# Kernel tuning notes

Measured on AMD Instinct MI355X. Metric: run time of the kernel, lower is better.

The kernel has to match this reference:

```python
import jax, jax.numpy as jnp
import numpy as np

D_MODEL = 1024
NUM_HEADS = 16
D_K = D_MODEL // NUM_HEADS
D_FF = 4096
THETA = 10000.0
EPS = 1e-5
B, S = 4, 2048


def _trunc_normal(key, shape, fan_in, fan_out):
    std = (2.0 / (fan_in + fan_out)) ** 0.5
    return jax.random.truncated_normal(key, -3.0, 3.0, shape, jnp.float32) * std


def setup_inputs() -> dict:
    key = jax.random.key(0)
    ks = jax.random.split(key, 8)
    return {
        "x": jax.random.normal(ks[0], (B, S, D_MODEL), jnp.float32),
        "wq": _trunc_normal(ks[1], (D_MODEL, D_MODEL), D_MODEL, D_MODEL),
        "wk": _trunc_normal(ks[2], (D_MODEL, D_MODEL), D_MODEL, D_MODEL),
        "wv": _trunc_normal(ks[3], (D_MODEL, D_MODEL), D_MODEL, D_MODEL),
        "wo": _trunc_normal(ks[4], (D_MODEL, D_MODEL), D_MODEL, D_MODEL),
        "g1": jnp.ones((D_MODEL,), jnp.float32),
        "g2": jnp.ones((D_MODEL,), jnp.float32),
        "w1": _trunc_normal(ks[5], (D_FF, D_MODEL), D_MODEL, D_FF),
        "w2": _trunc_normal(ks[6], (D_MODEL, D_FF), D_FF, D_MODEL),
        "w3": _trunc_normal(ks[7], (D_FF, D_MODEL), D_MODEL, D_FF),
    }


def _rmsnorm(x, g):
    rms = jnp.sqrt(jnp.mean(x * x, axis=-1, keepdims=True) + EPS)
    return x / rms * g


def _rope(x):
    # x: [b, h, s, d_k], interleaved rotary embedding
    s = x.shape[-2]
    inv_freq = 1.0 / (THETA ** (jnp.arange(0, D_K, 2, dtype=jnp.float32) / D_K))
    angles = jnp.arange(s, dtype=jnp.float32)[:, None] * inv_freq  # [s, d_k/2]
    cos, sin = jnp.cos(angles), jnp.sin(angles)
    x1, x2 = x[..., ::2], x[..., 1::2]
    rot = jnp.stack([x1 * cos - x2 * sin, x1 * sin + x2 * cos], axis=-1)
    return rot.reshape(x.shape)


def reference(x, wq, wk, wv, wo, g1, g2, w1, w2, w3):
    b, s, _ = x.shape
    h, dk = NUM_HEADS, D_K

    # --- attention sublayer ---
    xn = _rmsnorm(x, g1)
    q = (xn @ wq.T).reshape(b, s, h, dk).transpose(0, 2, 1, 3)
    k = (xn @ wk.T).reshape(b, s, h, dk).transpose(0, 2, 1, 3)
    v = (xn @ wv.T).reshape(b, s, h, dk).transpose(0, 2, 1, 3)
    q, k = _rope(q), _rope(k)

    scores = jnp.einsum("bhqd,bhkd->bhqk", q, k) / (dk ** 0.5)
    causal = jnp.tril(jnp.ones((s, s), dtype=bool))
    scores = jnp.where(causal, scores, -1e9)
    attn = jax.nn.softmax(scores, axis=-1)
    ctx = jnp.einsum("bhqk,bhkd->bhqd", attn, v)
    ctx = ctx.transpose(0, 2, 1, 3).reshape(b, s, h * dk)
    y = x + ctx @ wo.T

    # --- SwiGLU FFN sublayer ---
    yn = _rmsnorm(y, g2)
    a = yn @ w1.T
    ff = (a * jax.nn.sigmoid(a)) * (yn @ w3.T)
    return y + ff @ w2.T
```

## Files before the change

### kernel.cpp

```cpp
#include <hip/hip_runtime.h>
#include <hip/hip_bf16.h>

typedef unsigned short u16;
typedef unsigned int u32;
typedef __bf16 bf16_8 __attribute__((ext_vector_type(8)));
typedef float f32x4 __attribute__((ext_vector_type(4)));

#define DEV __device__ __forceinline__

static const int T_TOK = 8192;
static const int DM    = 1024;
static const int SEQ   = 2048;

DEV u16 f2b(float f) {
  union { float f; u32 u; } v; v.f = f;
  u32 r = v.u + 0x7fffu + ((v.u >> 16) & 1u);
  return (u16)(r >> 16);
}
DEV float b2f(u16 b) {
  union { u32 u; float f; } v; v.u = ((u32)b) << 16;
  return v.f;
}
DEV void gload16(void* lds, const void* g) {
  __builtin_amdgcn_global_load_lds((const __attribute__((address_space(1))) u32*)g,
                                   (__attribute__((address_space(3))) u32*)lds, 16, 0, 0);
}
DEV void vmdrain() { asm volatile("s_waitcnt vmcnt(0)" ::: "memory"); }
DEV uint2 tr_read(u32 addr) {
  uint2 r;
  asm volatile("ds_read_b64_tr_b16 %0, %1" : "=v"(r) : "v"(addr));
  return r;
}

__global__ void cvt_bf16(const float* __restrict__ in, u16* __restrict__ out, int n) {
  int i = (blockIdx.x * blockDim.x + threadIdx.x) * 4;
  if (i >= n) return;
  float4 v = *(const float4*)(in + i);
  union { u16 h[4]; uint2 u; } pk;
  pk.h[0] = f2b(v.x); pk.h[1] = f2b(v.y); pk.h[2] = f2b(v.z); pk.h[3] = f2b(v.w);
  *(uint2*)(out + i) = pk.u;
}

__launch_bounds__(256)
__global__ void rmsnorm_k(const float* __restrict__ x, const float* __restrict__ g,
                          u16* __restrict__ out) {
  const int row = blockIdx.x;
  const float4 v = ((const float4*)(x + (size_t)row * DM))[threadIdx.x];
  float ss = v.x*v.x + v.y*v.y + v.z*v.z + v.w*v.w;
  #pragma unroll
  for (int off = 1; off < 64; off <<= 1) ss += __shfl_xor(ss, off, 64);
  __shared__ float ws[4];
  if ((threadIdx.x & 63) == 0) ws[threadIdx.x >> 6] = ss;
  __syncthreads();
  float tot = ws[0] + ws[1] + ws[2] + ws[3];
  float inv = rsqrtf(tot * (1.0f / DM) + 1e-5f);
  const float4 gv = ((const float4*)g)[threadIdx.x];
  union { u16 h[4]; uint2 u; } pk;
  pk.h[0] = f2b(v.x * inv * gv.x);
  pk.h[1] = f2b(v.y * inv * gv.y);
  pk.h[2] = f2b(v.z * inv * gv.z);
  pk.h[3] = f2b(v.w * inv * gv.w);
  *(uint2*)(out + (size_t)row * DM + threadIdx.x * 4) = pk.u;
}

__global__ void rope_k(u16* __restrict__ buf, float scale) {
  int idx = blockIdx.x * blockDim.x + threadIdx.x;
  if (idx >= T_TOK * 512) return;
  int t = idx >> 9;
  int p = idx & 511;
  int d = p & 31;
  int s = t & (SEQ - 1);
  float inv = __expf(-(float)d * (logf(10000.0f) / 32.0f));
  float ang = (float)s * inv;
  float sn = sinf(ang), cs = cosf(ang);
  size_t off = (size_t)t * DM + (size_t)(p >> 5) * 64 + 2 * d;
  float x1 = b2f(buf[off]), x2 = b2f(buf[off + 1]);
  buf[off]     = f2b((x1 * cs - x2 * sn) * scale);
  buf[off + 1] = f2b((x1 * sn + x2 * cs) * scale);
}

template<int MODE>
__launch_bounds__(256)
__global__ void gemm_nt(const u16* __restrict__ A, const u16* __restrict__ B,
                        u16* Cb, float* __restrict__ Cf,
                        const float* __restrict__ resid, const u16* aux,
                        int N, int K) {
  __shared__ __attribute__((aligned(16))) u16 As[128 * 32];
  __shared__ __attribute__((aligned(16))) u16 Bs[128 * 32];
  const int tid = threadIdx.x;
  const int w = tid >> 6, l = tid & 63;
  const int wr = w >> 1, wc = w & 1;
  const int nwg = gridDim.x * gridDim.y;
  const int id  = blockIdx.y * gridDim.x + blockIdx.x;
  const int nid = (id & 7) * (nwg >> 3) + (id >> 3);
  const int bx = nid % gridDim.x, by = nid / gridDim.x;
  const int brow = by * 128;
  const int bcol = bx * 128;
  const int lr = l & 15, lg = l >> 4, lk = lg * 8;
  f32x4 acc[4][4] = {};

  for (int kk = 0; kk < K; kk += 32) {
    {
      int c = tid;
      gload16((char*)As + (size_t)w * 1024,
              A + (size_t)(brow + (c >> 2)) * K + kk + (c & 3) * 8);
      gload16((char*)Bs + (size_t)w * 1024,
              B + (size_t)(bcol + (c >> 2)) * K + kk + (c & 3) * 8);
      c = tid + 256;
      gload16((char*)As + 4096 + (size_t)w * 1024,
              A + (size_t)(brow + (c >> 2)) * K + kk + (c & 3) * 8);
      gload16((char*)Bs + 4096 + (size_t)w * 1024,
              B + (size_t)(bcol + (c >> 2)) * K + kk + (c & 3) * 8);
    }
    vmdrain();
    __syncthreads();
    bf16_8 af[4], bf[4];
    #pragma unroll
    for (int m = 0; m < 4; ++m)
      af[m] = *(const bf16_8*)&As[(wr * 64 + m * 16 + lr) * 32 + lk];
    #pragma unroll
    for (int n = 0; n < 4; ++n)
      bf[n] = *(const bf16_8*)&Bs[(wc * 64 + n * 16 + lr) * 32 + lk];
    #pragma unroll
    for (int m = 0; m < 4; ++m)
      #pragma unroll
      for (int n = 0; n < 4; ++n)
        acc[m][n] = __builtin_amdgcn_mfma_f32_16x16x32_bf16(af[m], bf[n], acc[m][n], 0, 0, 0);
    __syncthreads();
  }

  #pragma unroll
  for (int m = 0; m < 4; ++m) {
    #pragma unroll
    for (int n = 0; n < 4; ++n) {
      #pragma unroll
      for (int r = 0; r < 4; ++r) {
        int row = brow + wr * 64 + m * 16 + lg * 4 + r;
        int col = bcol + wc * 64 + n * 16 + lr;
        size_t idx = (size_t)row * N + col;
        float v = acc[m][n][r];
        if (MODE == 0) {
          Cb[idx] = f2b(v);
        } else if (MODE == 1 || MODE == 3) {
          Cf[idx] = resid[idx] + v;
        } else if (MODE == 2) {
          float av = b2f(aux[idx]);
          float sig = 1.0f / (1.0f + __expf(-av));
          Cb[idx] = f2b(av * sig * v);
        }
      }
    }
  }
}

__launch_bounds__(256)
__global__ void attn_k(const u16* __restrict__ Q, const u16* __restrict__ Kb,
                       const u16* __restrict__ V, u16* __restrict__ CTX) {
  __shared__ __attribute__((aligned(16))) u16 Ks[64 * 64];
  __shared__ __attribute__((aligned(16))) u16 Vs[64 * 64];
  __shared__ __attribute__((aligned(16))) u16 Ps[4][16 * 64];
  const int tid = threadIdx.x, w = tid >> 6, l = tid & 63;
  const int bh = blockIdx.y;
  const int b = bh >> 4, h = bh & 15;
  const int lr = l & 15, lg = l >> 4;
  const size_t base = (size_t)b * SEQ * DM + (size_t)h * 64;
  const u32 vs_base = (u32)(size_t)&Vs[0];

  #pragma unroll 1
  for (int pass = 0; pass < 2; ++pass) {
    const int qt = pass ? (31 - blockIdx.x) : blockIdx.x;
    const int q0 = qt * 64;

    const size_t qrow = base + (size_t)(q0 + w * 16 + lr) * DM;
    bf16_8 qf0 = *(const bf16_8*)&Q[qrow + lg * 8];
    bf16_8 qf1 = *(const bf16_8*)&Q[qrow + 32 + lg * 8];

    f32x4 o[4] = {};
    float mrow[4], lsum[4];
    #pragma unroll
    for (int r = 0; r < 4; ++r) { mrow[r] = -3.0e38f; lsum[r] = 0.0f; }

    for (int kv0 = 0; kv0 < q0 + 64; kv0 += 64) {
      __syncthreads();
      {
        int u = tid, row = u >> 3, slot = u & 7;
        gload16((char*)Ks + (size_t)w * 1024,
                Kb + base + (size_t)(kv0 + row) * DM + ((slot * 8) ^ ((row & 7) << 3)));
        u = tid + 256; row = u >> 3; slot = u & 7;
        gload16((char*)Ks + 4096 + (size_t)w * 1024,
                Kb + base + (size_t)(kv0 + row) * DM + ((slot * 8) ^ ((row & 7) << 3)));
        u = tid;
        int kv = ((u >> 5) << 2) + ((u >> 1) & 3);
        int d  = (((u >> 3) & 3) << 4) + ((u & 1) << 3);
        gload16((char*)Vs + (size_t)w * 1024,
                V + base + (size_t)(kv0 + kv) * DM + d);
        u = tid + 256;
        kv = ((u >> 5) << 2) + ((u >> 1) & 3);
        d  = (((u >> 3) & 3) << 4) + ((u & 1) << 3);
        gload16((char*)Vs + 4096 + (size_t)w * 1024,
                V + base + (size_t)(kv0 + kv) * DM + d);
      }
      vmdrain();
      __syncthreads();

      f32x4 s[4];
      #pragma unroll
      for (int h0 = 0; h0 < 4; ++h0) {
        const int row = h0 * 16 + lr;
        bf16_8 k0 = *(const bf16_8*)&Ks[row * 64 + ((lg * 8) ^ ((lr & 7) << 3))];
        bf16_8 k1 = *(const bf16_8*)&Ks[row * 64 + ((32 + lg * 8) ^ ((lr & 7) << 3))];
        f32x4 z = {};
        z = __builtin_amdgcn_mfma_f32_16x16x32_bf16(qf0, k0, z, 0, 0, 0);
        z = __builtin_amdgcn_mfma_f32_16x16x32_bf16(qf1, k1, z, 0, 0, 0);
        s[h0] = z;
      }

      #pragma unroll
      for (int r = 0; r < 4; ++r) {
        const int qg = q0 + w * 16 + lg * 4 + r;
        #pragma unroll
        for (int h0 = 0; h0 < 4; ++h0) {
          int kg = kv0 + h0 * 16 + lr;
          if (kg > qg) s[h0][r] = -3.0e38f;
        }
        float vmax = fmaxf(fmaxf(s[0][r], s[1][r]), fmaxf(s[2][r], s[3][r]));
        #pragma unroll
        for (int off = 1; off < 16; off <<= 1) vmax = fmaxf(vmax, __shfl_xor(vmax, off, 64));
        float mnew = fmaxf(mrow[r], vmax);
        float alpha = __expf(mrow[r] - mnew);
        mrow[r] = mnew;
        float p[4], rs = 0.0f;
        #pragma unroll
        for (int h0 = 0; h0 < 4; ++h0) { p[h0] = __expf(s[h0][r] - mnew); rs += p[h0]; }
        #pragma unroll
        for (int off = 1; off < 16; off <<= 1) rs += __shfl_xor(rs, off, 64);
        lsum[r] = lsum[r] * alpha + rs;
        o[0][r] *= alpha; o[1][r] *= alpha; o[2][r] *= alpha; o[3][r] *= alpha;
        const int ql = lg * 4 + r;
        #pragma unroll
        for (int h0 = 0; h0 < 4; ++h0)
          Ps[w][ql * 64 + (((h0 * 16 + lr) ^ ((ql & 7) << 3)))] = f2b(p[h0]);
      }

      #pragma unroll
      for (int kc = 0; kc < 2; ++kc) {
        bf16_8 pf = *(const bf16_8*)&Ps[w][lr * 64 + (((kc * 32 + lg * 8) ^ ((lr & 7) << 3)))];
        uint2 t0[4], t1[4];
        #pragma unroll
        for (int n = 0; n < 4; ++n) {
          u32 a0 = vs_base + (u32)((((kc * 8 + lg * 2 + 0) * 4 + n) * 128) + lr * 8);
          u32 a1 = vs_base + (u32)((((kc * 8 + lg * 2 + 1) * 4 + n) * 128) + lr * 8);
          t0[n] = tr_read(a0);
          t1[n] = tr_read(a1);
        }
        asm volatile("s_waitcnt lgkmcnt(0)" ::: "memory");
        __builtin_amdgcn_sched_barrier(0);
        #pragma unroll
        for (int n = 0; n < 4; ++n) {
          union { uint2 u2[2]; bf16_8 v; } vf;
          vf.u2[0] = t0[n]; vf.u2[1] = t1[n];
          o[n] = __builtin_amdgcn_mfma_f32_16x16x32_bf16(pf, vf.v, o[n], 0, 0, 0);
        }
      }
    }

    #pragma unroll
    for (int r = 0; r < 4; ++r) {
      float inv = 1.0f / lsum[r];
      size_t row = (size_t)b * SEQ + q0 + w * 16 + lg * 4 + r;
      #pragma unroll
      for (int n = 0; n < 4; ++n)
        CTX[row * DM + h * 64 + n * 16 + lr] = f2b(o[n][r] * inv);
    }
  }
}

extern "C" void kernel_launch(void* const* d_in, const int* in_sizes, int n_in,
                              void* d_out, int out_size, void* d_ws, size_t ws_size,
                              hipStream_t stream) {
  const float* x  = (const float*)d_in[0];
  const float* wq = (const float*)d_in[1];
  const float* wk = (const float*)d_in[2];
  const float* wv = (const float*)d_in[3];
  const float* wo = (const float*)d_in[4];
  const float* g1 = (const float*)d_in[5];
  const float* g2 = (const float*)d_in[6];
  const float* w1 = (const float*)d_in[7];
  const float* w2 = (const float*)d_in[8];
  const float* w3 = (const float*)d_in[9];

  char* ws = (char*)d_ws;
  const size_t MB = 1024 * 1024;
  u16*  WQb  = (u16*)(ws +  0 * MB);
  u16*  WKb  = (u16*)(ws +  2 * MB);
  u16*  WVb  = (u16*)(ws +  4 * MB);
  u16*  WOb  = (u16*)(ws +  6 * MB);
  u16*  W1b  = (u16*)(ws +  8 * MB);
  u16*  W3b  = (u16*)(ws + 16 * MB);
  u16*  W2b  = (u16*)(ws + 24 * MB);
  u16*  XN   = (u16*)(ws + 32 * MB);
  u16*  Qb   = (u16*)(ws + 48 * MB);
  u16*  Kb   = (u16*)(ws + 64 * MB);
  u16*  Vb   = (u16*)(ws + 80 * MB);
  u16*  CTX  = (u16*)(ws + 96 * MB);
  float* Y   = (float*)(ws + 112 * MB);
  u16*  FFIN = (u16*)(ws + 48 * MB);

  cvt_bf16<<<1024, 256, 0, stream>>>(wq, WQb, 1048576);
  cvt_bf16<<<1024, 256, 0, stream>>>(wk, WKb, 1048576);
  cvt_bf16<<<1024, 256, 0, stream>>>(wv, WVb, 1048576);
  cvt_bf16<<<1024, 256, 0, stream>>>(wo, WOb, 1048576);
  cvt_bf16<<<4096, 256, 0, stream>>>(w1, W1b, 4194304);
  cvt_bf16<<<4096, 256, 0, stream>>>(w3, W3b, 4194304);
  cvt_bf16<<<4096, 256, 0, stream>>>(w2, W2b, 4194304);

  rmsnorm_k<<<T_TOK, 256, 0, stream>>>(x, g1, XN);

  gemm_nt<0><<<dim3(8, 64), 256, 0, stream>>>(XN, WQb, Qb, nullptr, nullptr, nullptr, 1024, 1024);
  gemm_nt<0><<<dim3(8, 64), 256, 0, stream>>>(XN, WKb, Kb, nullptr, nullptr, nullptr, 1024, 1024);
  gemm_nt<0><<<dim3(8, 64), 256, 0, stream>>>(XN, WVb, Vb, nullptr, nullptr, nullptr, 1024, 1024);

  rope_k<<<16384, 256, 0, stream>>>(Qb, 0.125f);
  rope_k<<<16384, 256, 0, stream>>>(Kb, 1.0f);

  attn_k<<<dim3(16, 64), 256, 0, stream>>>(Qb, Kb, Vb, CTX);

  gemm_nt<1><<<dim3(8, 64), 256, 0, stream>>>(CTX, WOb, nullptr, Y, x, nullptr, 1024, 1024);

  rmsnorm_k<<<T_TOK, 256, 0, stream>>>(Y, g2, XN);

  gemm_nt<0><<<dim3(32, 64), 256, 0, stream>>>(XN, W1b, FFIN, nullptr, nullptr, nullptr, 4096, 1024);
  gemm_nt<2><<<dim3(32, 64), 256, 0, stream>>>(XN, W3b, FFIN, nullptr, nullptr, FFIN, 4096, 1024);

  gemm_nt<3><<<dim3(8, 64), 256, 0, stream>>>(FFIN, W2b, nullptr, (float*)d_out, Y, nullptr, 1024, 4096);
}
```

Measured before the change: 774.2 us.

## Swizzle GEMM LDS layout and fuse Q/K/V projections into one launch

The global-to-LDS load now XOR-swizzles the 16-byte chunk index per row, and the fragment reads apply the matching swizzle, so the MFMA operand reads from LDS hit fewer bank conflicts. The three separate Q, K and V projection GEMMs become a single gemm_qkv launch with a 24x64 grid, where each block picks its weight and output by column group. This removes two launches and tail effects, and gives the launch enough blocks to fill the GPU better. The swizzle has to match exactly between the store and load side, or the results will be wrong.

```diff
diff --git a/kernel.cpp b/kernel.cpp
--- a/kernel.cpp
+++ b/kernel.cpp
@@ -79,6 +79,38 @@
   buf[off + 1] = f2b((x1 * sn + x2 * cs) * scale);
 }
 
+
+#define GEMM_STAGE(As, Bs, Ap, Bp, K)                                          \
+  {                                                                            \
+    int c = tid;                                                               \
+    gload16((char*)As + (size_t)w * 1024,                                      \
+            Ap + (size_t)(brow + (c >> 2)) * K + kk + (((c & 3) ^ ((c >> 3) & 3)) << 3)); \
+    gload16((char*)Bs + (size_t)w * 1024,                                      \
+            Bp + (size_t)(bcol + (c >> 2)) * K + kk + (((c & 3) ^ ((c >> 3) & 3)) << 3)); \
+    c = tid + 256;                                                             \
+    gload16((char*)As + 4096 + (size_t)w * 1024,                               \
+            Ap + (size_t)(brow + (c >> 2)) * K + kk + (((c & 3) ^ ((c >> 3) & 3)) << 3)); \
+    gload16((char*)Bs + 4096 + (size_t)w * 1024,                               \
+            Bp + (size_t)(bcol + (c >> 2)) * K + kk + (((c & 3) ^ ((c >> 3) & 3)) << 3)); \
+  }
+
+#define GEMM_MFMA(As, Bs)                                                      \
+  {                                                                            \
+    const int swz = ((lr >> 1) & 3) ^ lg;                                      \
+    bf16_8 af[4], bfr[4];                                                      \
+    _Pragma("unroll")                                                          \
+    for (int m = 0; m < 4; ++m)                                                \
+      af[m] = *(const bf16_8*)&As[(wr * 64 + m * 16 + lr) * 32 + (swz << 3)];  \
+    _Pragma("unroll")                                                          \
+    for (int n = 0; n < 4; ++n)                                                \
+      bfr[n] = *(const bf16_8*)&Bs[(wc * 64 + n * 16 + lr) * 32 + (swz << 3)]; \
+    _Pragma("unroll")                                                          \
+    for (int m = 0; m < 4; ++m)                                                \
+      _Pragma("unroll")                                                        \
+      for (int n = 0; n < 4; ++n)                                              \
+        acc[m][n] = __builtin_amdgcn_mfma_f32_16x16x32_bf16(af[m], bfr[n], acc[m][n], 0, 0, 0); \
+  }
+
 template<int MODE>
 __launch_bounds__(256)
 __global__ void gemm_nt(const u16* __restrict__ A, const u16* __restrict__ B,
@@ -96,36 +128,14 @@
   const int bx = nid % gridDim.x, by = nid / gridDim.x;
   const int brow = by * 128;
   const int bcol = bx * 128;
-  const int lr = l & 15, lg = l >> 4, lk = lg * 8;
+  const int lr = l & 15, lg = l >> 4;
   f32x4 acc[4][4] = {};
 
   for (int kk = 0; kk < K; kk += 32) {
-    {
-      int c = tid;
-      gload16((char*)As + (size_t)w * 1024,
-              A + (size_t)(brow + (c >> 2)) * K + kk + (c & 3) * 8);
-      gload16((char*)Bs + (size_t)w * 1024,
-              B + (size_t)(bcol + (c >> 2)) * K + kk + (c & 3) * 8);
-      c = tid + 256;
-      gload16((char*)As + 4096 + (size_t)w * 1024,
-              A + (size_t)(brow + (c >> 2)) * K + kk + (c & 3) * 8);
-      gload16((char*)Bs + 4096 + (size_t)w * 1024,
-              B + (size_t)(bcol + (c >> 2)) * K + kk + (c & 3) * 8);
-    }
+    GEMM_STAGE(As, Bs, A, B, K)
     vmdrain();
     __syncthreads();
-    bf16_8 af[4], bf[4];
-    #pragma unroll
-    for (int m = 0; m < 4; ++m)
-      af[m] = *(const bf16_8*)&As[(wr * 64 + m * 16 + lr) * 32 + lk];
-    #pragma unroll
-    for (int n = 0; n < 4; ++n)
-      bf[n] = *(const bf16_8*)&Bs[(wc * 64 + n * 16 + lr) * 32 + lk];
-    #pragma unroll
-    for (int m = 0; m < 4; ++m)
-      #pragma unroll
-      for (int n = 0; n < 4; ++n)
-        acc[m][n] = __builtin_amdgcn_mfma_f32_16x16x32_bf16(af[m], bf[n], acc[m][n], 0, 0, 0);
+    GEMM_MFMA(As, Bs)
     __syncthreads();
   }
 
@@ -151,6 +161,50 @@
       }
     }
   }
+}
+
+__launch_bounds__(256)
+__global__ void gemm_qkv(const u16* __restrict__ A,
+                         const u16* __restrict__ Bq, const u16* __restrict__ Bk,
+                         const u16* __restrict__ Bv,
+                         u16* __restrict__ Oq, u16* __restrict__ Ok,
+                         u16* __restrict__ Ov) {
+  __shared__ __attribute__((aligned(16))) u16 As[128 * 32];
+  __shared__ __attribute__((aligned(16))) u16 Bs[128 * 32];
+  const int tid = threadIdx.x;
+  const int w = tid >> 6, l = tid & 63;
+  const int wr = w >> 1, wc = w & 1;
+  const int nwg = gridDim.x * gridDim.y;
+  const int id  = blockIdx.y * gridDim.x + blockIdx.x;
+  const int nid = (id & 7) * (nwg >> 3) + (id >> 3);
+  const int bx = nid % gridDim.x, by = nid / gridDim.x;
+  const int brow = by * 128;
+  const int mi = bx >> 3;
+  const int bcol = (bx & 7) * 128;
+  const u16* B = (mi == 0) ? Bq : (mi == 1) ? Bk : Bv;
+  u16* O = (mi == 0) ? Oq : (mi == 1) ? Ok : Ov;
+  const int lr = l & 15, lg = l >> 4;
+  const int K = 1024;
+  f32x4 acc[4][4] = {};
+
+  for (int kk = 0; kk < K; kk += 32) {
+    GEMM_STAGE(As, Bs, A, B, K)
+    vmdrain();
+    __syncthreads();
+    GEMM_MFMA(As, Bs)
+    __syncthreads();
+  }
+
+  #pragma unroll
+  for (int m = 0; m < 4; ++m)
+    #pragma unroll
+    for (int n = 0; n < 4; ++n)
+      #pragma unroll
+      for (int r = 0; r < 4; ++r) {
+        int row = brow + wr * 64 + m * 16 + lg * 4 + r;
+        int col = bcol + wc * 64 + n * 16 + lr;
+        O[(size_t)row * 1024 + col] = f2b(acc[m][n][r]);
+      }
 }
 
 __launch_bounds__(256)
@@ -316,9 +370,7 @@
 
   rmsnorm_k<<<T_TOK, 256, 0, stream>>>(x, g1, XN);
 
-  gemm_nt<0><<<dim3(8, 64), 256, 0, stream>>>(XN, WQb, Qb, nullptr, nullptr, nullptr, 1024, 1024);
-  gemm_nt<0><<<dim3(8, 64), 256, 0, stream>>>(XN, WKb, Kb, nullptr, nullptr, nullptr, 1024, 1024);
-  gemm_nt<0><<<dim3(8, 64), 256, 0, stream>>>(XN, WVb, Vb, nullptr, nullptr, nullptr, 1024, 1024);
+  gemm_qkv<<<dim3(24, 64), 256, 0, stream>>>(XN, WQb, WKb, WVb, Qb, Kb, Vb);
 
   rope_k<<<16384, 256, 0, stream>>>(Qb, 0.125f);
   rope_k<<<16384, 256, 0, stream>>>(Kb, 1.0f);
```

Result: faster. 750.5 us (-3.1%).
